# Optimization experiments

Hardware: AMD Instinct MI355X
Metric: run time of the kernel (lower is better)

Reference implementation:

```python
import jax, jax.numpy as jnp
import numpy as np

K = 4  # top-k from init
BN_IS_FOLDED = True  # BatchNorm (eval mode) folded into per-channel scale s and shift t


def tconv(x, W):
    # x: (b, C, v, n); W: (Cout, Cin, 3) temporal conv, kernel (3,1,1), padding (1,0,0), no bias
    return jax.lax.conv_general_dilated(
        x, W[:, :, :, None], window_strides=(1, 1),
        padding=((1, 1), (0, 0)), dimension_numbers=('NCHW', 'OIHW', 'NCHW'))


def gcn_single(xn, src, dst, Wg, bg):
    # PyG GCNConv: add self-loops, symmetric normalization, then scatter-add.
    N = xn.shape[0]
    xl = xn @ Wg  # (N, C)
    loop = jnp.arange(N, dtype=src.dtype)
    s = jnp.concatenate([src, loop])
    d = jnp.concatenate([dst, loop])
    deg = jax.ops.segment_sum(jnp.ones(s.shape[0], dtype=xn.dtype), d, num_segments=N)
    dinv = jnp.where(deg > 0, jax.lax.rsqrt(deg), 0.0)
    norm = dinv[s] * dinv[d]
    out = jax.ops.segment_sum(norm[:, None] * xl[s], d, num_segments=N)
    return out + bg


def setup_inputs() -> dict:
    key = jax.random.key(0)
    ks = jax.random.split(key, 10)
    C = 256
    x = jax.random.normal(ks[0], (512, C, 16, 16), dtype=jnp.float32)
    Wd = jax.random.normal(ks[1], (C, C, 3), dtype=jnp.float32) * 0.02
    s1 = 1.0 + 0.1 * jax.random.normal(ks[2], (C,), dtype=jnp.float32)
    t1 = 0.1 * jax.random.normal(ks[3], (C,), dtype=jnp.float32)
    Wg = jax.random.normal(ks[4], (C, C), dtype=jnp.float32) * 0.02
    bg = 0.01 * jax.random.normal(ks[5], (C,), dtype=jnp.float32)
    Wu = jax.random.normal(ks[6], (C, C, 3), dtype=jnp.float32) * 0.02
    s2 = 1.0 + 0.1 * jax.random.normal(ks[7], (C,), dtype=jnp.float32)
    t2 = 0.1 * jax.random.normal(ks[8], (C,), dtype=jnp.float32)
    return {"x": x, "batch": 4, "Wd": Wd, "s1": s1, "t1": t1,
            "Wg": Wg, "bg": bg, "Wu": Wu, "s2": s2, "t2": t2}


def reference(x, batch, Wd, s1, t1, Wg, bg, Wu, s2, t2):
    tlen, c, h, w = x.shape
    b = batch
    v = tlen // b
    hw = h * w
    # (tlen,c,h,w) -> (b,c,v,h*w)
    x4 = x.reshape(b, v, c, h, w).transpose(0, 2, 1, 3, 4).reshape(b, c, v, hw)
    xd = tconv(x4, Wd) * s1[None, :, None, None] + t1[None, :, None, None]  # down_conv + BN(eval)

    # --- dynamic graph build (no-grad in original) ---
    f = jax.lax.stop_gradient(xd).transpose(0, 2, 3, 1)  # (b, v, hw, c)
    f1, f2 = f[:, :-1], f[:, 1:]                          # (b, t_1, hw, c)
    t_1 = v - 1
    sq1 = jnp.sum(f1 * f1, axis=-1)                       # (b,t_1,hw)
    sq2 = jnp.sum(f2 * f2, axis=-1)
    dots = jnp.einsum('btnc,btmc->btnm', f1, f2)
    d2 = jnp.maximum(sq1[..., :, None] + sq2[..., None, :] - 2.0 * dots, 0.0)
    sim = -jnp.sqrt(d2).reshape(b, t_1, hw * hw)
    sim = sim / jnp.maximum(jnp.linalg.norm(sim, axis=-1, keepdims=True), 1e-12)  # F.normalize
    sim = jnp.where(sim < 0.05, 100.0, sim)
    _, idx = jax.lax.top_k(sim, K)                        # (b, t_1, K)
    frame = jnp.arange(t_1, dtype=jnp.int32)[None, :, None]
    row = (idx // hw).astype(jnp.int32) + frame * hw
    col = (idx % hw).astype(jnp.int32) + (frame + 1) * hw
    row = row.reshape(b, -1)
    col = col.reshape(b, -1)
    src = jnp.concatenate([row, col], axis=1)             # forward + reversed edges
    dst = jnp.concatenate([col, row], axis=1)

    # --- per-sample GCN (batched with vmap) ---
    nodes = xd.transpose(0, 2, 3, 1).reshape(b, v * hw, c)  # 'b c v n -> b (v n) c'
    out = jax.vmap(lambda xn, s, d: gcn_single(xn, s, d, Wg, bg))(nodes, src, dst)

    # --- up path ---
    o4 = out.transpose(0, 2, 1).reshape(b, c, v, hw)
    xu = tconv(o4, Wu) * s2[None, :, None, None] + t2[None, :, None, None]
    return xu.reshape(b, c, v, h, w).transpose(0, 2, 1, 3, 4).reshape(tlen, c, h, w)
```

## Files before the change

kernel.cpp:

```cpp
#include <hip/hip_runtime.h>

typedef __attribute__((ext_vector_type(8))) short short8;
typedef __attribute__((ext_vector_type(4))) float f32x4;
typedef unsigned short u16;
typedef unsigned int u32;

#define FENCE() asm volatile("" ::: "memory")

__device__ __forceinline__ void gld_lds16(const void* g, void* l) {
  __builtin_amdgcn_global_load_lds((const __attribute__((address_space(1))) void*)g,
                                   (__attribute__((address_space(3))) void*)l,
                                   16, 0, 0);
}

__device__ __forceinline__ u16 f2b(float x) {
  union { float f; u32 u; } v; v.f = x;
  u32 u = v.u;
  return (u16)((u + 0x7FFFu + ((u >> 16) & 1u)) >> 16);
}
__device__ __forceinline__ float b2f(u16 x) {
  union { u32 u; float f; } v; v.u = ((u32)x) << 16; return v.f;
}
__device__ __forceinline__ u32 pack_pair(float lo, float hi) {
  return (u32)f2b(lo) | ((u32)f2b(hi) << 16);
}

__global__ __launch_bounds__(256) void k_prep(const float* __restrict__ Wd, const float* __restrict__ Wg,
                                              const float* __restrict__ Wu,
                                              const float* __restrict__ s1, const float* __restrict__ t1,
                                              const float* __restrict__ bg,
                                              u16* __restrict__ WdT, u16* __restrict__ Wup,
                                              u16* __restrict__ WgS,
                                              float* __restrict__ c0, float* __restrict__ tWg) {
  int blk = blockIdx.x;
  int tid = threadIdx.x;
  if (blk == 1024) {
    int j = tid;
    float a = 0.f;
    for (int co = 0; co < 256; ++co) a += t1[co] * Wg[co * 256 + j];
    tWg[j] = a;
    c0[j] = a + bg[j];
    return;
  }
  int id = blk * 256 + tid;
  if (id < 196608) {
    int kk = id >> 16;
    int rem = id & 65535;
    int a = rem >> 8, b = rem & 255;
    Wup[id] = f2b(Wu[(u32)a * 768 + (u32)b * 3 + kk]);
    WdT[id] = f2b(Wd[(u32)b * 768 + (u32)a * 3 + kk]);
  } else {
    int id2 = id - 196608;
    int j = id2 >> 8, co = id2 & 255;
    WgS[id2] = f2b(Wg[co * 256 + j] * s1[co]);
  }
}

__global__ __launch_bounds__(256) void k_zero(u16* __restrict__ outz, u16* __restrict__ xTz) {
  int gid = blockIdx.x * 256 + threadIdx.x;
  int i = gid * 8;
  int buf = (i >= 327680) ? 1 : 0;
  int wi = i - buf * 327680;
  int f = wi >> 16;
  int off = wi & 65535;
  u16* dst = (buf ? xTz : outz) + (size_t)f * 129 * 65536 + off;
  *(uint4*)dst = make_uint4(0u, 0u, 0u, 0u);
}

__global__ __launch_bounds__(256) void k_transpose(const float* __restrict__ x, u16* __restrict__ xTz) {
  __shared__ u16 tile[64][72];
  int blk = blockIdx.x;
  int tl = blk >> 4;
  int sub = blk & 15;
  int ci0 = (sub >> 2) << 6;
  int p0 = (sub & 3) << 6;
  int tid = threadIdx.x;
  int i = tid >> 2;
  int ch = tid & 3;
  const float* gsrc = x + (size_t)tl * 65536 + (ci0 + i) * 256 + p0 + ch * 16;
  __align__(16) u16 cv[16];
#pragma unroll
  for (int v4 = 0; v4 < 4; ++v4) {
    float4 f = *(const float4*)(gsrc + v4 * 4);
    cv[v4 * 4 + 0] = f2b(f.x);
    cv[v4 * 4 + 1] = f2b(f.y);
    cv[v4 * 4 + 2] = f2b(f.z);
    cv[v4 * 4 + 3] = f2b(f.w);
  }
  *(uint4*)&tile[i][ch * 16] = *(const uint4*)&cv[0];
  *(uint4*)&tile[i][ch * 16 + 8] = *(const uint4*)&cv[8];
  __syncthreads();
  __align__(16) u16 tmp[16];
#pragma unroll
  for (int cc = 0; cc < 16; ++cc) tmp[cc] = tile[ch * 16 + cc][i];
  int fi = (tl >> 7) * 129 + (tl & 127) + 1;
  u16* gdst = xTz + (size_t)fi * 65536 + (p0 + i) * 256 + ci0 + ch * 16;
  *(uint4*)(gdst) = *(const uint4*)&tmp[0];
  *(uint4*)(gdst + 8) = *(const uint4*)&tmp[8];
}

__device__ __forceinline__ void stage_tile(const u16* __restrict__ g, int ldg, u16* s, int w, int lane) {
  int r = lane >> 2;
  int cc = (lane & 3) * 8;
#pragma unroll
  for (int j = 0; j < 2; ++j) {
    gld_lds16(g + (w * 32 + j * 16 + r) * ldg + cc, s + (w * 32 + j * 16) * 32);
  }
}

__device__ __forceinline__ void mfma_tiles(const u16* sA, const u16* sB, f32x4 acc[4][4],
                                           int wr, int wc, int lane) {
  int m16 = lane & 15;
  int q8 = (lane >> 4) * 8;
  short8 a[4], b[4];
#pragma unroll
  for (int mi = 0; mi < 4; ++mi) a[mi] = *(const short8*)(sA + (wr * 64 + mi * 16 + m16) * 32 + q8);
#pragma unroll
  for (int ni = 0; ni < 4; ++ni) b[ni] = *(const short8*)(sB + (wc * 64 + ni * 16 + m16) * 32 + q8);
#pragma unroll
  for (int mi = 0; mi < 4; ++mi)
#pragma unroll
    for (int ni = 0; ni < 4; ++ni)
      acc[mi][ni] = __builtin_amdgcn_mfma_f32_16x16x32_bf16(a[mi], b[ni], acc[mi][ni], 0, 0, 0);
}

__device__ __forceinline__ void store_pairs(u16* base, int row0, int stride, int colb,
                                            const float v[4], bool ev) {
  float pv[4];
#pragma unroll
  for (int r = 0; r < 4; ++r) pv[r] = __shfl_xor(v[r], 1, 64);
  u32 wd0 = ev ? pack_pair(v[0], pv[0]) : pack_pair(pv[0], v[0]);
  u32 wd1 = ev ? pack_pair(v[1], pv[1]) : pack_pair(pv[1], v[1]);
  u32 wd2 = ev ? pack_pair(v[2], pv[2]) : pack_pair(pv[2], v[2]);
  u32 wd3 = ev ? pack_pair(v[3], pv[3]) : pack_pair(pv[3], v[3]);
  u32 wa = ev ? wd0 : wd2;
  u32 wb = ev ? wd1 : wd3;
  int rs = ev ? 0 : 2;
  *(u32*)(base + (size_t)(row0 + rs) * stride + colb) = wa;
  *(u32*)(base + (size_t)(row0 + rs + 1) * stride + colb) = wb;
}

__device__ __forceinline__ void store_pairs_f32(float* base, int row0, int stride, int colb,
                                                const float v[4], bool ev) {
  float pv[4];
#pragma unroll
  for (int r = 0; r < 4; ++r) pv[r] = __shfl_xor(v[r], 1, 64);
  float2 wa, wb;
  if (ev) { wa = make_float2(v[0], pv[0]); wb = make_float2(v[1], pv[1]); }
  else    { wa = make_float2(pv[2], v[2]); wb = make_float2(pv[3], v[3]); }
  int rs = ev ? 0 : 2;
  *(float2*)(base + (size_t)(row0 + rs) * stride + colb) = wa;
  *(float2*)(base + (size_t)(row0 + rs + 1) * stride + colb) = wb;
}

__global__ __launch_bounds__(256) void k_wcomb(const u16* __restrict__ WgS, const u16* __restrict__ WdT,
                                               u16* __restrict__ Wcomb) {
  __shared__ u16 sA[128 * 32];
  __shared__ u16 sB[128 * 32];
  int blk = blockIdx.x;
  int kk = blk >> 2;
  int tile = blk & 3;
  int tm = tile >> 1, tn = tile & 1;
  int tid = threadIdx.x, lane = tid & 63, w = tid >> 6;
  int wr = w >> 1, wc = w & 1;
  f32x4 acc[4][4];
#pragma unroll
  for (int i = 0; i < 4; ++i)
#pragma unroll
    for (int j = 0; j < 4; ++j) acc[i][j] = (f32x4){0.f, 0.f, 0.f, 0.f};
  const u16* gA = WgS + (size_t)(tm * 128) * 256;
  const u16* gB = WdT + (size_t)kk * 65536 + (size_t)(tn * 128) * 256;
  for (int ks = 0; ks < 8; ++ks) {
    stage_tile(gA + ks * 32, 256, sA, w, lane);
    stage_tile(gB + ks * 32, 256, sB, w, lane);
    __syncthreads();
    mfma_tiles(sA, sB, acc, wr, wc, lane);
    __syncthreads();
  }
  int q = lane >> 4, c = lane & 15;
  bool ev = (lane & 1) == 0;
  u16* obase = Wcomb + (size_t)kk * 65536;
#pragma unroll
  for (int mi = 0; mi < 4; ++mi) {
    int row0 = tm * 128 + wr * 64 + mi * 16 + q * 4;
#pragma unroll
    for (int ni = 0; ni < 4; ++ni) {
      float v[4];
#pragma unroll
      for (int r = 0; r < 4; ++r) v[r] = acc[mi][ni][r];
      int colb = tn * 128 + wc * 64 + ni * 16 + (c & ~1);
      store_pairs(obase, row0, 256, colb, v, ev);
    }
  }
}


__device__ __forceinline__ void stage_part(int s, const u16* Ab, const u16* Bb,
                                           u16* sA, u16* sB, int wuni, int g0) {
  if (s >= 48) return;
  const int tau = s >> 2;
  const int pt = s & 3;
  const int toff = ((tau >> 2) << 16) + ((tau & 3) << 6);
  const int half = pt & 1;
  const u16* src = ((pt & 2) ? Ab : Bb) + toff + (half << 15) + g0;
  u16* dst = ((pt & 2) ? sA : sB) + ((tau & 1) << 14) + (half << 13) + wuni;
  gld_lds16(src, dst);
  gld_lds16(src + 16384, dst + 4096);
}

template<int QUAD, int NH>
__device__ __forceinline__ void mfma_quad(f32x4 (&acc)[8][4], const short8 (&af)[2][4],
                                          const short8 (&bf)[2][2][2]) {
#pragma unroll
  for (int k = 0; k < 2; ++k)
#pragma unroll
    for (int m = 0; m < 4; ++m)
#pragma unroll
      for (int nj = 0; nj < 2; ++nj)
        acc[QUAD * 4 + m][NH * 2 + nj] = __builtin_amdgcn_mfma_f32_16x16x32_bf16(
            af[k][m], bf[NH][k][nj], acc[QUAD * 4 + m][NH * 2 + nj], 0, 0, 0);
}

__device__ __forceinline__ void gemm256_core(const u16* __restrict__ Ab, const u16* __restrict__ Bb,
                                             u16* sA, u16* sB, int tid, f32x4 (&acc)[8][4]) {
  const int lane = tid & 63;
  const int w = tid >> 6;
  const int wr = w >> 2;
  const int wc = w & 3;
  const int m16 = lane & 15;
  const int xorm = (lane & 7) << 4;
  const int q16b = (lane >> 4) << 4;
  const int koffe0 = ((q16b) ^ xorm) >> 1;
  const int koffe1 = ((64 + q16b) ^ xorm) >> 1;
  const int srow = tid >> 3;
  const int scol = ((tid & 7) ^ (srow & 7)) << 3;
  const int g0 = srow * 256 + scol;
  const int wuni = w << 9;

#pragma unroll
  for (int i = 0; i < 8; ++i)
#pragma unroll
    for (int j = 0; j < 4; ++j) acc[i][j] = (f32x4){0.f, 0.f, 0.f, 0.f};

#pragma unroll
  for (int s = 0; s < 7; ++s) stage_part(s, Ab, Bb, sA, sB, wuni, g0);
  asm volatile("s_waitcnt vmcnt(6)" ::: "memory");
  __builtin_amdgcn_s_barrier();
  FENCE();

  short8 af[2][4];
  short8 bf[2][2][2];
#pragma unroll 2
  for (int kt = 0; kt < 12; ++kt) {
    const int cb = kt & 1;
    const u16* aH = sA + cb * 16384 + wr * 8192;
    const u16* bH = sB + cb * 16384 + (wc >> 1) * 8192;
    const int bR0 = (wc & 1) << 6;
#pragma unroll
    for (int m = 0; m < 4; ++m) {
      const u16* p = aH + (m * 16 + m16) * 64;
      af[0][m] = *(const short8*)(p + koffe0);
      af[1][m] = *(const short8*)(p + koffe1);
    }
#pragma unroll
    for (int nh = 0; nh < 2; ++nh)
#pragma unroll
      for (int nj = 0; nj < 2; ++nj) {
        const u16* p = bH + (bR0 + (nh * 2 + nj) * 16 + m16) * 64;
        bf[nh][0][nj] = *(const short8*)(p + koffe0);
        bf[nh][1][nj] = *(const short8*)(p + koffe1);
      }
    stage_part(4 * kt + 7, Ab, Bb, sA, sB, wuni, g0);
    FENCE();
    __builtin_amdgcn_s_barrier();
    FENCE();
    __builtin_amdgcn_s_setprio(1);
    mfma_quad<0, 0>(acc, af, bf);
    __builtin_amdgcn_s_setprio(0);
    FENCE();
    __builtin_amdgcn_s_barrier();
    FENCE();
    stage_part(4 * kt + 8, Ab, Bb, sA, sB, wuni, g0);
    FENCE();
    __builtin_amdgcn_s_barrier();
    FENCE();
    __builtin_amdgcn_s_setprio(1);
    mfma_quad<0, 1>(acc, af, bf);
    __builtin_amdgcn_s_setprio(0);
    FENCE();
    __builtin_amdgcn_s_barrier();
    FENCE();
#pragma unroll
    for (int m = 0; m < 4; ++m) {
      const u16* p = aH + (64 + m * 16 + m16) * 64;
      af[0][m] = *(const short8*)(p + koffe0);
      af[1][m] = *(const short8*)(p + koffe1);
    }
    stage_part(4 * kt + 9, Ab, Bb, sA, sB, wuni, g0);
    FENCE();
    __builtin_amdgcn_s_barrier();
    FENCE();
    __builtin_amdgcn_s_setprio(1);
    mfma_quad<1, 0>(acc, af, bf);
    __builtin_amdgcn_s_setprio(0);
    FENCE();
    __builtin_amdgcn_s_barrier();
    FENCE();
    stage_part(4 * kt + 10, Ab, Bb, sA, sB, wuni, g0);
    FENCE();
    __builtin_amdgcn_s_barrier();
    FENCE();
    __builtin_amdgcn_s_setprio(1);
    mfma_quad<1, 1>(acc, af, bf);
    __builtin_amdgcn_s_setprio(0);
    if (kt < 10) asm volatile("s_waitcnt vmcnt(6)" ::: "memory");
    else         asm volatile("s_waitcnt vmcnt(0)" ::: "memory");
    __builtin_amdgcn_s_barrier();
    FENCE();
  }
}

__global__ __launch_bounds__(512, 2) void k_g12(const u16* __restrict__ xTz, const u16* __restrict__ Wcomb,
                                                const float* __restrict__ c0, const float* __restrict__ tWg,
                                                u16* __restrict__ outz, float* __restrict__ edge) {
  __shared__ u16 sA[32768];
  __shared__ u16 sB[32768];
  int bsw = (int)blockIdx.x;
  int bt = (bsw & 7) * 64 + (bsw >> 3);
  int b = bt >> 7, t = bt & 127;
  int tid = threadIdx.x;
  const u16* Ab = xTz + (size_t)(b * 129 + t) * 65536;
  const u16* Bb = Wcomb;
  f32x4 acc[8][4];
  gemm256_core(Ab, Bb, sA, sB, tid, acc);

  int lane = tid & 63, w = tid >> 6, wr = w >> 2, wc = w & 3;
  int q = lane >> 4, cc16 = lane & 15;
  bool ev = (lane & 1) == 0;
  float c0v[4], tWgv[4];
#pragma unroll
  for (int ni = 0; ni < 4; ++ni) {
    int j = wc * 64 + ni * 16 + cc16;
    c0v[ni] = c0[j];
    tWgv[ni] = tWg[j];
  }
  u16* obase = outz + (size_t)(b * 129 + t + 1) * 65536;
#pragma unroll
  for (int mi = 0; mi < 8; ++mi) {
    int row0 = wr * 128 + mi * 16 + q * 4;
#pragma unroll
    for (int ni = 0; ni < 4; ++ni) {
      float v[4];
#pragma unroll
      for (int r = 0; r < 4; ++r) v[r] = acc[mi][ni][r] + c0v[ni];
      store_pairs(obase, row0, 256, wc * 64 + ni * 16 + (cc16 & ~1), v, ev);
    }
  }
  if (wr == 0 && q == 0) {
    float* eb = edge + (size_t)bt * 1024;
#pragma unroll
    for (int ni = 0; ni < 4; ++ni) {
      float vE[4];
#pragma unroll
      for (int r = 0; r < 4; ++r) vE[r] = acc[0][ni][r] + tWgv[ni];
      store_pairs_f32(eb, 0, 256, wc * 64 + ni * 16 + (cc16 & ~1), vE, ev);
    }
  }
}

__device__ __forceinline__ float dinv0(int t) {
  if (t == 0) return 0.44721359549995793f;
  if (t == 127) return 0.7071067811865476f;
  return 0.4082482904638631f;
}
__global__ __launch_bounds__(256) void k_fix(const float* __restrict__ edge, const float* __restrict__ bg,
                                             u16* __restrict__ outz) {
  int bt = blockIdx.x;
  int b = bt >> 7;
  int t = bt & 127;
  int j = threadIdx.x;
  const float ISQ2 = 0.7071067811865476f;
  float bgv = bg[j];
  float e_t = edge[(size_t)bt * 1024 + j];
  float At = dinv0(t);
  float o0 = bgv + At * At * e_t;
  if (t <= 126) {
    float At1 = dinv0(t + 1);
    const float* en = edge + (size_t)(bt + 1) * 1024;
    float s = At1 * en[j] + ISQ2 * (en[256 + j] + en[512 + j] + en[768 + j]);
    o0 += At * s;
  }
  float em1 = 0.f, Atm1 = 0.f;
  if (t >= 1) {
    Atm1 = dinv0(t - 1);
    em1 = edge[(size_t)(bt - 1) * 1024 + j];
    o0 += At * Atm1 * em1;
  }
  u16* ob = outz + (size_t)(b * 129 + t + 1) * 65536;
  ob[j] = f2b(o0);
#pragma unroll
  for (int k = 1; k <= 3; ++k) {
    float m = edge[(size_t)bt * 1024 + k * 256 + j];
    float ok = (t == 0) ? (bgv + m) : (bgv + 0.5f * m + ISQ2 * Atm1 * em1);
    ob[k * 256 + j] = f2b(ok);
  }
}

__global__ __launch_bounds__(512, 2) void k_g3(const u16* __restrict__ outz, const u16* __restrict__ Wup,
                                               const float* __restrict__ s2, const float* __restrict__ t2,
                                               float* __restrict__ y) {
  __shared__ u16 sA[32768];
  __shared__ u16 sB[32768];
  int bsw = (int)blockIdx.x;
  int bt = (bsw & 7) * 64 + (bsw >> 3);
  int b = bt >> 7, t = bt & 127;
  int tid = threadIdx.x;
  const u16* Ab = Wup;
  const u16* Bb = outz + (size_t)(b * 129 + t) * 65536;
  f32x4 acc[8][4];
  gemm256_core(Ab, Bb, sA, sB, tid, acc);

  int lane = tid & 63, w = tid >> 6, wr = w >> 2, wc = w & 3;
  int q = lane >> 4, cc16 = lane & 15;
  bool ev = (lane & 1) == 0;
  float* ybase = y + (size_t)bt * 65536;
#pragma unroll
  for (int mi = 0; mi < 8; ++mi) {
    int rl = wr * 128 + mi * 16 + q * 4;
    float4 s4 = *(const float4*)(s2 + rl);
    float4 t4 = *(const float4*)(t2 + rl);
#pragma unroll
    for (int ni = 0; ni < 4; ++ni) {
      float v[4];
      v[0] = acc[mi][ni][0] * s4.x + t4.x;
      v[1] = acc[mi][ni][1] * s4.y + t4.y;
      v[2] = acc[mi][ni][2] * s4.z + t4.z;
      v[3] = acc[mi][ni][3] * s4.w + t4.w;
      store_pairs_f32(ybase, rl, 256, wc * 64 + ni * 16 + (cc16 & ~1), v, ev);
    }
  }
}

extern "C" void kernel_launch(void* const* d_in, const int* in_sizes, int n_in,
                              void* d_out, int out_size, void* d_ws, size_t ws_size,
                              hipStream_t stream) {
  (void)in_sizes; (void)n_in; (void)out_size; (void)ws_size;
  const float* x  = (const float*)d_in[0];
  const float* Wd = (const float*)d_in[2];
  const float* s1 = (const float*)d_in[3];
  const float* t1 = (const float*)d_in[4];
  const float* Wg = (const float*)d_in[5];
  const float* bg = (const float*)d_in[6];
  const float* Wu = (const float*)d_in[7];
  const float* s2 = (const float*)d_in[8];
  const float* t2 = (const float*)d_in[9];
  float* y = (float*)d_out;
  char* ws = (char*)d_ws;
  u16*   outz  = (u16*)(ws);
  u16*   xTz   = (u16*)(ws + 67764224);
  u16*   WdT   = (u16*)(ws + 135528448);
  u16*   WgS   = (u16*)(ws + 135921664);
  u16*   Wup   = (u16*)(ws + 136052736);
  u16*   Wcomb = (u16*)(ws + 136445952);
  float* c0    = (float*)(ws + 136839168);
  float* tWg   = (float*)(ws + 136840192);
  float* edge  = (float*)d_out;

  k_prep<<<dim3(1025), dim3(256), 0, stream>>>(Wd, Wg, Wu, s1, t1, bg, WdT, Wup, WgS, c0, tWg);
  k_wcomb<<<dim3(12), dim3(256), 0, stream>>>(WgS, WdT, Wcomb);
  k_zero<<<dim3(320), dim3(256), 0, stream>>>(outz, xTz);
  k_transpose<<<dim3(8192), dim3(256), 0, stream>>>(x, xTz);
  k_g12<<<dim3(512), dim3(512), 0, stream>>>(xTz, Wcomb, c0, tWg, outz, edge);
  k_fix<<<dim3(512), dim3(256), 0, stream>>>(edge, bg, outz);
  k_g3<<<dim3(512), dim3(512), 0, stream>>>(outz, Wup, s2, t2, y);
}
```

Baseline: 398.4 us.

## Merge prep kernels into one launch and restructure GEMM main-loop pipeline

New measurement: 446.4 us. 1.12x slower.

```diff
diff --git a/kernel.cpp b/kernel.cpp
--- a/kernel.cpp
+++ b/kernel.cpp
@@ -25,16 +25,69 @@
   return (u32)f2b(lo) | ((u32)f2b(hi) << 16);
 }
 
-__global__ __launch_bounds__(256) void k_prep(const float* __restrict__ Wd, const float* __restrict__ Wg,
-                                              const float* __restrict__ Wu,
-                                              const float* __restrict__ s1, const float* __restrict__ t1,
-                                              const float* __restrict__ bg,
-                                              u16* __restrict__ WdT, u16* __restrict__ Wup,
-                                              u16* __restrict__ WgS,
-                                              float* __restrict__ c0, float* __restrict__ tWg) {
+__global__ __launch_bounds__(256) void k_pre(const float* __restrict__ x,
+                                             const float* __restrict__ Wd, const float* __restrict__ Wg,
+                                             const float* __restrict__ Wu,
+                                             const float* __restrict__ s1, const float* __restrict__ t1,
+                                             const float* __restrict__ bg,
+                                             u16* __restrict__ xTz, u16* __restrict__ outz,
+                                             u16* __restrict__ Wup, u16* __restrict__ Wcomb,
+                                             float* __restrict__ c0, float* __restrict__ tWg) {
+  __shared__ u16 tile[64][72];
   int blk = blockIdx.x;
   int tid = threadIdx.x;
-  if (blk == 1024) {
+  if (blk < 8192) {
+    int tl = blk >> 4;
+    int sub = blk & 15;
+    int ci0 = (sub >> 2) << 6;
+    int p0 = (sub & 3) << 6;
+    int i = tid >> 2;
+    int ch = tid & 3;
+    const float* gsrc = x + (size_t)tl * 65536 + (ci0 + i) * 256 + p0 + ch * 16;
+    __align__(16) u16 cv[16];
+#pragma unroll
+    for (int v4 = 0; v4 < 4; ++v4) {
+      float4 f = *(const float4*)(gsrc + v4 * 4);
+      cv[v4 * 4 + 0] = f2b(f.x);
+      cv[v4 * 4 + 1] = f2b(f.y);
+      cv[v4 * 4 + 2] = f2b(f.z);
+      cv[v4 * 4 + 3] = f2b(f.w);
+    }
+    *(uint4*)&tile[i][ch * 16] = *(const uint4*)&cv[0];
+    *(uint4*)&tile[i][ch * 16 + 8] = *(const uint4*)&cv[8];
+    __syncthreads();
+    __align__(16) u16 tmp[16];
+#pragma unroll
+    for (int cc = 0; cc < 16; ++cc) tmp[cc] = tile[ch * 16 + cc][i];
+    int fi = (tl >> 7) * 129 + (tl & 127) + 1;
+    u16* gdst = xTz + (size_t)fi * 65536 + (p0 + i) * 256 + ci0 + ch * 16;
+    *(uint4*)(gdst) = *(const uint4*)&tmp[0];
+    *(uint4*)(gdst + 8) = *(const uint4*)&tmp[8];
+    return;
+  }
+  if (blk < 8960) {
+    int r = blk - 8192;
+    int kk = r >> 8;
+    int ci = r & 255;
+    int j = tid;
+    float a = 0.f;
+    for (int co = 0; co < 256; ++co) {
+      float wv = b2f(f2b(Wg[co * 256 + j] * s1[co]));
+      float dv = b2f(f2b(Wd[(u32)co * 768 + (u32)ci * 3 + kk]));
+      a = fmaf(wv, dv, a);
+    }
+    Wcomb[(size_t)kk * 65536 + (size_t)j * 256 + ci] = f2b(a);
+    return;
+  }
+  if (blk < 9728) {
+    int id = (blk - 8960) * 256 + tid;
+    int kk = id >> 16;
+    int rem = id & 65535;
+    int a = rem >> 8, b = rem & 255;
+    Wup[id] = f2b(Wu[(u32)a * 768 + (u32)b * 3 + kk]);
+    return;
+  }
+  if (blk == 9728) {
     int j = tid;
     float a = 0.f;
     for (int co = 0; co < 256; ++co) a += t1[co] * Wg[co * 256 + j];
@@ -42,22 +95,7 @@
     c0[j] = a + bg[j];
     return;
   }
-  int id = blk * 256 + tid;
-  if (id < 196608) {
-    int kk = id >> 16;
-    int rem = id & 65535;
-    int a = rem >> 8, b = rem & 255;
-    Wup[id] = f2b(Wu[(u32)a * 768 + (u32)b * 3 + kk]);
-    WdT[id] = f2b(Wd[(u32)b * 768 + (u32)a * 3 + kk]);
-  } else {
-    int id2 = id - 196608;
-    int j = id2 >> 8, co = id2 & 255;
-    WgS[id2] = f2b(Wg[co * 256 + j] * s1[co]);
-  }
-}
-
-__global__ __launch_bounds__(256) void k_zero(u16* __restrict__ outz, u16* __restrict__ xTz) {
-  int gid = blockIdx.x * 256 + threadIdx.x;
+  int gid = (blk - 9729) * 256 + tid;
   int i = gid * 8;
   int buf = (i >= 327680) ? 1 : 0;
   int wi = i - buf * 327680;
@@ -65,63 +103,6 @@
   int off = wi & 65535;
   u16* dst = (buf ? xTz : outz) + (size_t)f * 129 * 65536 + off;
   *(uint4*)dst = make_uint4(0u, 0u, 0u, 0u);
-}
-
-__global__ __launch_bounds__(256) void k_transpose(const float* __restrict__ x, u16* __restrict__ xTz) {
-  __shared__ u16 tile[64][72];
-  int blk = blockIdx.x;
-  int tl = blk >> 4;
-  int sub = blk & 15;
-  int ci0 = (sub >> 2) << 6;
-  int p0 = (sub & 3) << 6;
-  int tid = threadIdx.x;
-  int i = tid >> 2;
-  int ch = tid & 3;
-  const float* gsrc = x + (size_t)tl * 65536 + (ci0 + i) * 256 + p0 + ch * 16;
-  __align__(16) u16 cv[16];
-#pragma unroll
-  for (int v4 = 0; v4 < 4; ++v4) {
-    float4 f = *(const float4*)(gsrc + v4 * 4);
-    cv[v4 * 4 + 0] = f2b(f.x);
-    cv[v4 * 4 + 1] = f2b(f.y);
-    cv[v4 * 4 + 2] = f2b(f.z);
-    cv[v4 * 4 + 3] = f2b(f.w);
-  }
-  *(uint4*)&tile[i][ch * 16] = *(const uint4*)&cv[0];
-  *(uint4*)&tile[i][ch * 16 + 8] = *(const uint4*)&cv[8];
-  __syncthreads();
-  __align__(16) u16 tmp[16];
-#pragma unroll
-  for (int cc = 0; cc < 16; ++cc) tmp[cc] = tile[ch * 16 + cc][i];
-  int fi = (tl >> 7) * 129 + (tl & 127) + 1;
-  u16* gdst = xTz + (size_t)fi * 65536 + (p0 + i) * 256 + ci0 + ch * 16;
-  *(uint4*)(gdst) = *(const uint4*)&tmp[0];
-  *(uint4*)(gdst + 8) = *(const uint4*)&tmp[8];
-}
-
-__device__ __forceinline__ void stage_tile(const u16* __restrict__ g, int ldg, u16* s, int w, int lane) {
-  int r = lane >> 2;
-  int cc = (lane & 3) * 8;
-#pragma unroll
-  for (int j = 0; j < 2; ++j) {
-    gld_lds16(g + (w * 32 + j * 16 + r) * ldg + cc, s + (w * 32 + j * 16) * 32);
-  }
-}
-
-__device__ __forceinline__ void mfma_tiles(const u16* sA, const u16* sB, f32x4 acc[4][4],
-                                           int wr, int wc, int lane) {
-  int m16 = lane & 15;
-  int q8 = (lane >> 4) * 8;
-  short8 a[4], b[4];
-#pragma unroll
-  for (int mi = 0; mi < 4; ++mi) a[mi] = *(const short8*)(sA + (wr * 64 + mi * 16 + m16) * 32 + q8);
-#pragma unroll
-  for (int ni = 0; ni < 4; ++ni) b[ni] = *(const short8*)(sB + (wc * 64 + ni * 16 + m16) * 32 + q8);
-#pragma unroll
-  for (int mi = 0; mi < 4; ++mi)
-#pragma unroll
-    for (int ni = 0; ni < 4; ++ni)
-      acc[mi][ni] = __builtin_amdgcn_mfma_f32_16x16x32_bf16(a[mi], b[ni], acc[mi][ni], 0, 0, 0);
 }
 
 __device__ __forceinline__ void store_pairs(u16* base, int row0, int stride, int colb,
@@ -153,72 +134,14 @@
   *(float2*)(base + (size_t)(row0 + rs + 1) * stride + colb) = wb;
 }
 
-__global__ __launch_bounds__(256) void k_wcomb(const u16* __restrict__ WgS, const u16* __restrict__ WdT,
-                                               u16* __restrict__ Wcomb) {
-  __shared__ u16 sA[128 * 32];
-  __shared__ u16 sB[128 * 32];
-  int blk = blockIdx.x;
-  int kk = blk >> 2;
-  int tile = blk & 3;
-  int tm = tile >> 1, tn = tile & 1;
-  int tid = threadIdx.x, lane = tid & 63, w = tid >> 6;
-  int wr = w >> 1, wc = w & 1;
-  f32x4 acc[4][4];
-#pragma unroll
-  for (int i = 0; i < 4; ++i)
-#pragma unroll
-    for (int j = 0; j < 4; ++j) acc[i][j] = (f32x4){0.f, 0.f, 0.f, 0.f};
-  const u16* gA = WgS + (size_t)(tm * 128) * 256;
-  const u16* gB = WdT + (size_t)kk * 65536 + (size_t)(tn * 128) * 256;
-  for (int ks = 0; ks < 8; ++ks) {
-    stage_tile(gA + ks * 32, 256, sA, w, lane);
-    stage_tile(gB + ks * 32, 256, sB, w, lane);
-    __syncthreads();
-    mfma_tiles(sA, sB, acc, wr, wc, lane);
-    __syncthreads();
-  }
-  int q = lane >> 4, c = lane & 15;
-  bool ev = (lane & 1) == 0;
-  u16* obase = Wcomb + (size_t)kk * 65536;
-#pragma unroll
-  for (int mi = 0; mi < 4; ++mi) {
-    int row0 = tm * 128 + wr * 64 + mi * 16 + q * 4;
-#pragma unroll
-    for (int ni = 0; ni < 4; ++ni) {
-      float v[4];
-#pragma unroll
-      for (int r = 0; r < 4; ++r) v[r] = acc[mi][ni][r];
-      int colb = tn * 128 + wc * 64 + ni * 16 + (c & ~1);
-      store_pairs(obase, row0, 256, colb, v, ev);
-    }
-  }
-}
-
-
-__device__ __forceinline__ void stage_part(int s, const u16* Ab, const u16* Bb,
-                                           u16* sA, u16* sB, int wuni, int g0) {
-  if (s >= 48) return;
-  const int tau = s >> 2;
-  const int pt = s & 3;
+
+__device__ __forceinline__ void stage_half(const u16* __restrict__ op, int tau, int half,
+                                           u16* sdst, int g0, int wuni) {
   const int toff = ((tau >> 2) << 16) + ((tau & 3) << 6);
-  const int half = pt & 1;
-  const u16* src = ((pt & 2) ? Ab : Bb) + toff + (half << 15) + g0;
-  u16* dst = ((pt & 2) ? sA : sB) + ((tau & 1) << 14) + (half << 13) + wuni;
+  const u16* src = op + toff + (half << 15) + g0;
+  u16* dst = sdst + ((tau & 1) << 14) + (half << 13) + wuni;
   gld_lds16(src, dst);
   gld_lds16(src + 16384, dst + 4096);
-}
-
-template<int QUAD, int NH>
-__device__ __forceinline__ void mfma_quad(f32x4 (&acc)[8][4], const short8 (&af)[2][4],
-                                          const short8 (&bf)[2][2][2]) {
-#pragma unroll
-  for (int k = 0; k < 2; ++k)
-#pragma unroll
-    for (int m = 0; m < 4; ++m)
-#pragma unroll
-      for (int nj = 0; nj < 2; ++nj)
-        acc[QUAD * 4 + m][NH * 2 + nj] = __builtin_amdgcn_mfma_f32_16x16x32_bf16(
-            af[k][m], bf[NH][k][nj], acc[QUAD * 4 + m][NH * 2 + nj], 0, 0, 0);
 }
 
 __device__ __forceinline__ void gemm256_core(const u16* __restrict__ Ab, const u16* __restrict__ Bb,
@@ -230,7 +153,7 @@
   const int m16 = lane & 15;
   const int xorm = (lane & 7) << 4;
   const int q16b = (lane >> 4) << 4;
-  const int koffe0 = ((q16b) ^ xorm) >> 1;
+  const int koffe0 = (q16b ^ xorm) >> 1;
   const int koffe1 = ((64 + q16b) ^ xorm) >> 1;
   const int srow = tid >> 3;
   const int scol = ((tid & 7) ^ (srow & 7)) << 3;
@@ -242,79 +165,74 @@
 #pragma unroll
     for (int j = 0; j < 4; ++j) acc[i][j] = (f32x4){0.f, 0.f, 0.f, 0.f};
 
-#pragma unroll
-  for (int s = 0; s < 7; ++s) stage_part(s, Ab, Bb, sA, sB, wuni, g0);
-  asm volatile("s_waitcnt vmcnt(6)" ::: "memory");
+  stage_half(Ab, 0, 0, sA, g0, wuni);
+  stage_half(Ab, 0, 1, sA, g0, wuni);
+  stage_half(Bb, 0, 0, sB, g0, wuni);
+  stage_half(Bb, 0, 1, sB, g0, wuni);
+  stage_half(Bb, 1, 0, sB, g0, wuni);
+  stage_half(Bb, 1, 1, sB, g0, wuni);
+  asm volatile("s_waitcnt vmcnt(4)" ::: "memory");
   __builtin_amdgcn_s_barrier();
   FENCE();
 
-  short8 af[2][4];
-  short8 bf[2][2][2];
+  short8 a0[4], a1[4], bf0[4], bf1[4];
 #pragma unroll 2
   for (int kt = 0; kt < 12; ++kt) {
-    const int cb = kt & 1;
-    const u16* aH = sA + cb * 16384 + wr * 8192;
-    const u16* bH = sB + cb * 16384 + (wc >> 1) * 8192;
+    const u16* aH = sA + (kt & 1) * 16384 + wr * 8192;
+    const u16* bH = sB + (kt & 1) * 16384 + (wc >> 1) * 8192;
     const int bR0 = (wc & 1) << 6;
 #pragma unroll
-    for (int m = 0; m < 4; ++m) {
-      const u16* p = aH + (m * 16 + m16) * 64;
-      af[0][m] = *(const short8*)(p + koffe0);
-      af[1][m] = *(const short8*)(p + koffe1);
-    }
-#pragma unroll
-    for (int nh = 0; nh < 2; ++nh)
-#pragma unroll
-      for (int nj = 0; nj < 2; ++nj) {
-        const u16* p = bH + (bR0 + (nh * 2 + nj) * 16 + m16) * 64;
-        bf[nh][0][nj] = *(const short8*)(p + koffe0);
-        bf[nh][1][nj] = *(const short8*)(p + koffe1);
-      }
-    stage_part(4 * kt + 7, Ab, Bb, sA, sB, wuni, g0);
+    for (int m = 0; m < 4; ++m) a0[m] = *(const short8*)(aH + (m * 16 + m16) * 64 + koffe0);
+#pragma unroll
+    for (int n = 0; n < 4; ++n) bf0[n] = *(const short8*)(bH + (bR0 + n * 16 + m16) * 64 + koffe0);
+    if (kt < 11) stage_half(Ab, kt + 1, 0, sA, g0, wuni);
+    __builtin_amdgcn_s_setprio(1);
+#pragma unroll
+    for (int m = 0; m < 4; ++m)
+#pragma unroll
+      for (int n = 0; n < 4; ++n)
+        acc[m][n] = __builtin_amdgcn_mfma_f32_16x16x32_bf16(a0[m], bf0[n], acc[m][n], 0, 0, 0);
+    __builtin_amdgcn_s_setprio(0);
+#pragma unroll
+    for (int m = 0; m < 4; ++m) a1[m] = *(const short8*)(aH + (m * 16 + m16) * 64 + koffe1);
+#pragma unroll
+    for (int n = 0; n < 4; ++n) bf1[n] = *(const short8*)(bH + (bR0 + n * 16 + m16) * 64 + koffe1);
+    if (kt < 11) stage_half(Ab, kt + 1, 1, sA, g0, wuni);
+    __builtin_amdgcn_s_setprio(1);
+#pragma unroll
+    for (int m = 0; m < 4; ++m)
+#pragma unroll
+      for (int n = 0; n < 4; ++n)
+        acc[m][n] = __builtin_amdgcn_mfma_f32_16x16x32_bf16(a1[m], bf1[n], acc[m][n], 0, 0, 0);
+    __builtin_amdgcn_s_setprio(0);
+    asm volatile("s_waitcnt lgkmcnt(0)" ::: "memory");
     FENCE();
     __builtin_amdgcn_s_barrier();
     FENCE();
+#pragma unroll
+    for (int m = 0; m < 4; ++m) a0[m] = *(const short8*)(aH + ((64 + m * 16) + m16) * 64 + koffe0);
+    if (kt < 10) stage_half(Bb, kt + 2, 0, sB, g0, wuni);
     __builtin_amdgcn_s_setprio(1);
-    mfma_quad<0, 0>(acc, af, bf);
+#pragma unroll
+    for (int m = 0; m < 4; ++m)
+#pragma unroll
+      for (int n = 0; n < 4; ++n)
+        acc[4 + m][n] = __builtin_amdgcn_mfma_f32_16x16x32_bf16(a0[m], bf0[n], acc[4 + m][n], 0, 0, 0);
     __builtin_amdgcn_s_setprio(0);
+#pragma unroll
+    for (int m = 0; m < 4; ++m) a1[m] = *(const short8*)(aH + ((64 + m * 16) + m16) * 64 + koffe1);
+    if (kt < 10) stage_half(Bb, kt + 2, 1, sB, g0, wuni);
+    __builtin_amdgcn_s_setprio(1);
+#pragma unroll
+    for (int m = 0; m < 4; ++m)
+#pragma unroll
+      for (int n = 0; n < 4; ++n)
+        acc[4 + m][n] = __builtin_amdgcn_mfma_f32_16x16x32_bf16(a1[m], bf1[n], acc[4 + m][n], 0, 0, 0);
+    __builtin_amdgcn_s_setprio(0);
+    asm volatile("s_waitcnt lgkmcnt(0)" ::: "memory");
+    if (kt < 10) asm volatile("s_waitcnt vmcnt(4)" ::: "memory");
+    else         asm volatile("s_waitcnt vmcnt(0)" ::: "memory");
     FENCE();
-    __builtin_amdgcn_s_barrier();
-    FENCE();
-    stage_part(4 * kt + 8, Ab, Bb, sA, sB, wuni, g0);
-    FENCE();
-    __builtin_amdgcn_s_barrier();
-    FENCE();
-    __builtin_amdgcn_s_setprio(1);
-    mfma_quad<0, 1>(acc, af, bf);
-    __builtin_amdgcn_s_setprio(0);
-    FENCE();
-    __builtin_amdgcn_s_barrier();
-    FENCE();
-#pragma unroll
-    for (int m = 0; m < 4; ++m) {
-      const u16* p = aH + (64 + m * 16 + m16) * 64;
-      af[0][m] = *(const short8*)(p + koffe0);
-      af[1][m] = *(const short8*)(p + koffe1);
-    }
-    stage_part(4 * kt + 9, Ab, Bb, sA, sB, wuni, g0);
-    FENCE();
-    __builtin_amdgcn_s_barrier();
-    FENCE();
-    __builtin_amdgcn_s_setprio(1);
-    mfma_quad<1, 0>(acc, af, bf);
-    __builtin_amdgcn_s_setprio(0);
-    FENCE();
-    __builtin_amdgcn_s_barrier();
-    FENCE();
-    stage_part(4 * kt + 10, Ab, Bb, sA, sB, wuni, g0);
-    FENCE();
-    __builtin_amdgcn_s_barrier();
-    FENCE();
-    __builtin_amdgcn_s_setprio(1);
-    mfma_quad<1, 1>(acc, af, bf);
-    __builtin_amdgcn_s_setprio(0);
-    if (kt < 10) asm volatile("s_waitcnt vmcnt(6)" ::: "memory");
-    else         asm volatile("s_waitcnt vmcnt(0)" ::: "memory");
     __builtin_amdgcn_s_barrier();
     FENCE();
   }
@@ -458,18 +376,13 @@
   char* ws = (char*)d_ws;
   u16*   outz  = (u16*)(ws);
   u16*   xTz   = (u16*)(ws + 67764224);
-  u16*   WdT   = (u16*)(ws + 135528448);
-  u16*   WgS   = (u16*)(ws + 135921664);
   u16*   Wup   = (u16*)(ws + 136052736);
   u16*   Wcomb = (u16*)(ws + 136445952);
   float* c0    = (float*)(ws + 136839168);
   float* tWg   = (float*)(ws + 136840192);
   float* edge  = (float*)d_out;
 
-  k_prep<<<dim3(1025), dim3(256), 0, stream>>>(Wd, Wg, Wu, s1, t1, bg, WdT, Wup, WgS, c0, tWg);
-  k_wcomb<<<dim3(12), dim3(256), 0, stream>>>(WgS, WdT, Wcomb);
-  k_zero<<<dim3(320), dim3(256), 0, stream>>>(outz, xTz);
-  k_transpose<<<dim3(8192), dim3(256), 0, stream>>>(x, xTz);
+  k_pre<<<dim3(10049), dim3(256), 0, stream>>>(x, Wd, Wg, Wu, s1, t1, bg, xTz, outz, Wup, Wcomb, c0, tWg);
   k_g12<<<dim3(512), dim3(512), 0, stream>>>(xTz, Wcomb, c0, tWg, outz, edge);
   k_fix<<<dim3(512), dim3(256), 0, stream>>>(edge, bg, outz);
   k_g3<<<dim3(512), dim3(512), 0, stream>>>(outz, Wup, s2, t2, y);
```
